# Performance work log

Measured on AMD Instinct MI355X. Metric: run time of the kernel, lower is better.

Reference implementation:

```python
import jax, jax.numpy as jnp
import numpy as np

T, B, L, CTX, H = 512, 512, 16, 64, 128
STATE_DIM, SHOT, PID, DATA = 32, 12, 35, 23


def setup_inputs() -> dict:
    key = jax.random.key(0)
    ks = jax.random.split(key, 64)
    k = iter(ks)
    def rn(shape, s=0.1):
        return (jax.random.normal(next(k), shape) * s).astype(jnp.float32)
    xs = jax.random.normal(next(k), (T, B, DATA), jnp.float32)
    xs = xs.at[:, :, 12].set(jax.random.randint(next(k), (T, B), 0, SHOT).astype(jnp.float32))
    xs = xs.at[:, :, 17].set(jax.random.randint(next(k), (T, B), 0, PID).astype(jnp.float32))
    xs = xs.at[:, :, 20].set(jax.random.randint(next(k), (T, B), 0, SHOT).astype(jnp.float32))
    return dict(
        total_xs=jnp.zeros((1,), jnp.float32),
        xs=xs,
        ts=jnp.linspace(0.0, 2.0, T).astype(jnp.float32),
        noise_std=jnp.asarray(0.1, jnp.float32),
        z0_noise=jax.random.normal(next(k), (B, L), jnp.float32),
        bm_noise=jax.random.normal(next(k), (T - 1, B, L), jnp.float32),
        shot_emb=rn((SHOT, 8)), player_emb=rn((PID, 8)),
        gru_wih=rn((3 * H, STATE_DIM)), gru_whh=rn((3 * H, H)),
        gru_bih=rn((3 * H,)), gru_bhh=rn((3 * H,)),
        enc_w=rn((CTX, H)), enc_b=rn((CTX,)),
        qz0_w=rn((2 * L, CTX)), qz0_b=rn((2 * L,)),
        f_w1=rn((H, L + CTX)), f_b1=rn((H,)), f_w2=rn((H, H)), f_b2=rn((H,)),
        f_w3=rn((L, H)), f_b3=rn((L,)),
        h_w1=rn((H, L)), h_b1=rn((H,)), h_w2=rn((H, H)), h_b2=rn((H,)),
        h_w3=rn((L, H)), h_b3=rn((L,)),
        g_w1=rn((L, H)), g_b1=rn((L, H)), g_w2=rn((L, H)), g_b2=rn((L,)),
        proj_w=rn((STATE_DIM, L)), proj_b=rn((STATE_DIM,)),
        pz0_mean=jnp.zeros((1, L), jnp.float32), pz0_logstd=jnp.zeros((1, L), jnp.float32),
        act_w=rn((128, L)), act_b=rn((128,)),
        act_land_w=rn((2, 128)), act_shot_w=rn((SHOT, 128)), act_move_w=rn((2, 128)),
    )


def _forward(xs, noise_std, shot_emb, player_emb, gru_wih, gru_whh, gru_bih, gru_bhh,
             enc_w, enc_b, qz0_w, qz0_b,
             f_w1, f_b1, f_w2, f_b2, f_w3, f_b3,
             h_w1, h_b1, h_w2, h_b2, h_w3, h_b3,
             g_w1, g_b1, g_w2, g_b2,
             proj_w, proj_b, pz0_mean, pz0_logstd,
             act_w, act_b, act_land_w, act_shot_w, act_move_w,
             ts, z0_noise, bm_noise):
    # --- SDE_embed_and_transform: replace shot/player id cols with embeddings ---
    state = xs[:, :, :18]
    shot_ids = state[:, :, 12].astype(jnp.int32)
    pid_ids = state[:, :, 17].astype(jnp.int32)
    state_t = jnp.concatenate([state[:, :, :12], shot_emb[shot_ids],
                               state[:, :, 13:17], player_emb[pid_ids]], axis=-1)  # (T,B,32)
    xs_t = jnp.concatenate([state_t, xs[:, :, 18:]], axis=-1)  # (T,B,37)
    # --- Encoder: GRU over time-reversed states, linear head, flip back ---
    def gru_step(h, xt):
        gi = xt @ gru_wih.T + gru_bih
        gh = h @ gru_whh.T + gru_bhh
        ir, iz, inn = jnp.split(gi, 3, axis=-1)
        hr, hz, hn = jnp.split(gh, 3, axis=-1)
        r = jax.nn.sigmoid(ir + hr)
        zg = jax.nn.sigmoid(iz + hz)
        n = jnp.tanh(inn + r * hn)
        hnew = (1.0 - zg) * n + zg * h
        return hnew, hnew
    h0 = jnp.zeros((xs.shape[1], gru_whh.shape[1]), xs.dtype)
    _, hs = jax.lax.scan(gru_step, h0, state_t[::-1])
    ctx = (hs @ enc_w.T + enc_b)[::-1]  # (T,B,CTX)
    # --- posterior z0 ---
    qm, qls = jnp.split(ctx[0] @ qz0_w.T + qz0_b, 2, axis=1)
    z0 = qm + jnp.exp(qls) * z0_noise
    # --- Euler-Maruyama with logqp; searchsorted(right) -> ctx[min(i+1,T-1)] = ctx[i+1] ---
    dts = ts[1:] - ts[:-1]  # (T-1,)
    dW = jnp.sqrt(dts)[:, None, None] * bm_noise
    ctx_steps = ctx[1:]
    def mlp3(x, w1, b1, w2, b2, w3, b3):
        h1 = jax.nn.softplus(x @ w1.T + b1)
        h2 = jax.nn.softplus(h1 @ w2.T + b2)
        return h2 @ w3.T + b3
    def g_diag(y):  # (B,L): per-latent-dim scalar nets, batched over L
        hg = jax.nn.softplus(y[:, :, None] * g_w1[None] + g_b1[None])  # (B,L,H)
        return jax.nn.sigmoid(jnp.einsum('blh,lh->bl', hg, g_w2) + g_b2)
    def sde_step(z, inp):
        c, dw, dt = inp
        f_val = mlp3(jnp.concatenate([z, c], axis=1), f_w1, f_b1, f_w2, f_b2, f_w3, f_b3)
        h_val = mlp3(z, h_w1, h_b1, h_w2, h_b2, h_w3, h_b3)
        g_val = g_diag(z)
        u = (f_val - h_val) / g_val
        logr = 0.5 * jnp.sum(u * u, axis=1) * dt
        z_new = z + f_val * dt + g_val * dw
        return z_new, (z_new, logr)
    _, (z_tail, log_ratio) = jax.lax.scan(sde_step, z0, (ctx_steps, dW, dts))
    zs = jnp.concatenate([z0[None], z_tail], axis=0)  # (T,B,L)
    _xs = zs @ proj_w.T + proj_b  # (T,B,32)
    # --- action model losses ---
    a = jax.nn.relu(zs @ act_w.T + act_b)
    land = (a @ act_land_w.T).reshape(-1, 2)
    shot_logits = (a @ act_shot_w.T).reshape(-1, act_shot_w.shape[0])
    move = (a @ act_move_w.T).reshape(-1, 2)
    true_actions = xs_t[:, :, -5:]
    true_land = true_actions[:, :, :2].reshape(-1, 2)
    true_move = true_actions[:, :, 3:].reshape(-1, 2)
    true_shot = true_actions[:, :, 2].astype(jnp.int32).reshape(-1)
    land_loss = jnp.mean((land - true_land) ** 2)
    move_loss = jnp.mean((move - true_move) ** 2)
    logp = jax.nn.log_softmax(shot_logits, axis=-1)
    picked = jnp.take_along_axis(logp, true_shot[:, None], axis=1)[:, 0]
    mask = (true_shot != 0).astype(logp.dtype)  # CrossEntropy ignore_index=0
    shot_loss = -jnp.sum(picked * mask) / jnp.maximum(jnp.sum(mask), 1.0)
    # --- reconstruction log-likelihood ---
    xs_state = xs_t[:, :, :STATE_DIM]
    LOG2PI = 1.8378770664093453
    log_pxs = jnp.mean(jnp.sum(
        -0.5 * ((xs_state - _xs) / noise_std) ** 2 - jnp.log(noise_std) - 0.5 * LOG2PI,
        axis=(0, 2)))
    # --- KL(q(z0) || p(z0)) ---
    var_q = jnp.exp(2.0 * qls)
    var_p = jnp.exp(2.0 * pz0_logstd)
    kl = pz0_logstd - qls + (var_q + (qm - pz0_mean) ** 2) / (2.0 * var_p) - 0.5
    logqp0 = jnp.mean(jnp.sum(kl, axis=1))
    logqp_path = jnp.mean(jnp.sum(log_ratio, axis=0))
    return log_pxs, logqp0 + logqp_path + land_loss + shot_loss + move_loss


def reference(total_xs, xs, ts, noise_std, z0_noise, bm_noise, shot_emb, player_emb,
              gru_wih, gru_whh, gru_bih, gru_bhh, enc_w, enc_b, qz0_w, qz0_b,
              f_w1, f_b1, f_w2, f_b2, f_w3, f_b3, h_w1, h_b1, h_w2, h_b2, h_w3, h_b3,
              g_w1, g_b1, g_w2, g_b2, proj_w, proj_b, pz0_mean, pz0_logstd,
              act_w, act_b, act_land_w, act_shot_w, act_move_w):
    return _forward(xs, noise_std, shot_emb, player_emb, gru_wih, gru_whh, gru_bih, gru_bhh,
                    enc_w, enc_b, qz0_w, qz0_b,
                    f_w1, f_b1, f_w2, f_b2, f_w3, f_b3,
                    h_w1, h_b1, h_w2, h_b2, h_w3, h_b3,
                    g_w1, g_b1, g_w2, g_b2,
                    proj_w, proj_b, pz0_mean, pz0_logstd,
                    act_w, act_b, act_land_w, act_shot_w, act_move_w,
                    ts, z0_noise, bm_noise)
```

## Files before the change

kernel.cpp:

```cpp
#include <hip/hip_runtime.h>
#include <cstdint>

typedef _Float16 f16;
typedef _Float16 f16x2 __attribute__((ext_vector_type(2)));

#define T_STEPS 512
#define B_SZ 512
#define LOG2PI 1.8378770664093453f

__device__ __forceinline__ uint32_t packh2(float a, float b) {
  f16x2 v; v[0] = (f16)a; v[1] = (f16)b;
  return __builtin_bit_cast(uint32_t, v);
}

__device__ __forceinline__ float fdot2(uint32_t a, uint32_t b, float c) {
#if defined(__AMDGCN__) && __has_builtin(__builtin_amdgcn_fdot2)
  return __builtin_amdgcn_fdot2(__builtin_bit_cast(f16x2, a),
                                __builtin_bit_cast(f16x2, b), c, false);
#else
  f16x2 x = __builtin_bit_cast(f16x2, a), y = __builtin_bit_cast(f16x2, b);
  return c + (float)x[0] * (float)y[0] + (float)x[1] * (float)y[1];
#endif
}

#define DOT4(acc, w0, w1, w2, w3, v)                                     \
  do {                                                                   \
    acc = fdot2((w0), (v).x, acc); acc = fdot2((w1), (v).y, acc);        \
    acc = fdot2((w2), (v).z, acc); acc = fdot2((w3), (v).w, acc);        \
  } while (0)

__device__ __forceinline__ float sigmoidf_(float x) {
  return 1.0f / (1.0f + __expf(-x));
}
__device__ __forceinline__ float tanhf_(float x) {
  float ax = fabsf(x);
  float t = __expf(-2.0f * ax);
  float r = (1.0f - t) / (1.0f + t);
  return copysignf(r, x);
}
__device__ __forceinline__ float softplusf_(float x) {
  return fmaxf(x, 0.0f) + __logf(1.0f + __expf(-fabsf(x)));
}

__global__ __launch_bounds__(256) void k_embed(
    const float* __restrict__ xs, const float* __restrict__ shot_emb,
    const float* __restrict__ player_emb, f16* __restrict__ state_t,
    float* __restrict__ accums) {
  if (blockIdx.x == 0 && threadIdx.x < 16) accums[threadIdx.x] = 0.0f;
  size_t idx = (size_t)blockIdx.x * 256 + threadIdx.x;
  const float* xp = xs + idx * 23;
  f16* op = state_t + idx * 32;
  int sid = (int)xp[12];
  int pid = (int)xp[17];
#pragma unroll
  for (int i = 0; i < 12; ++i) op[i] = (f16)xp[i];
  const float* se = shot_emb + sid * 8;
#pragma unroll
  for (int i = 0; i < 8; ++i) op[12 + i] = (f16)se[i];
#pragma unroll
  for (int i = 0; i < 4; ++i) op[20 + i] = (f16)xp[13 + i];
  const float* pe = player_emb + pid * 8;
#pragma unroll
  for (int i = 0; i < 8; ++i) op[24 + i] = (f16)pe[i];
}

__global__ __launch_bounds__(512) void k_gru(
    const f16* __restrict__ state_t, const float* __restrict__ wih,
    const float* __restrict__ whh, const float* __restrict__ bih,
    const float* __restrict__ bhh, const float* __restrict__ enc_w,
    const float* __restrict__ enc_b, const float* __restrict__ qz0_w,
    const float* __restrict__ qz0_b, const float* __restrict__ z0_noise,
    const float* __restrict__ pz0_mean, const float* __restrict__ pz0_logstd,
    f16* __restrict__ ctx, float* __restrict__ z0_out,
    float* __restrict__ accums) {
  __shared__ uint32_t s_x[2][16];
  __shared__ uint32_t s_h[2][64];
  __shared__ float s_gates[2 * 128 * 4];
  __shared__ float s_encp[2 * 64 * 2];
  __shared__ float s_ctx0[2][64];
  __shared__ float s_q[2][32];

  const int tid = threadIdx.x;
  const int bbase = blockIdx.x * 2;
  const uint32_t* stu = (const uint32_t*)state_t;

  uint32_t wA[64];
  uint32_t wB[16];
  float bias0 = 0.f, bias1 = 0.f, encbr = 0.f;

  if (tid < 256) {
    int g = tid >> 7, du = tid & 127;
    const float* whr = whh + (size_t)(g * 128 + du) * 128;
#pragma unroll
    for (int i = 0; i < 64; ++i) wA[i] = packh2(whr[2 * i], whr[2 * i + 1]);
    const float* wxr = wih + (size_t)(g * 128 + du) * 32;
#pragma unroll
    for (int i = 0; i < 16; ++i) wB[i] = packh2(wxr[2 * i], wxr[2 * i + 1]);
    bias0 = bih[g * 128 + du] + bhh[g * 128 + du];
  } else if (tid < 384) {
    int du = tid - 256;
    const float* whr = whh + (size_t)(256 + du) * 128;
#pragma unroll
    for (int i = 0; i < 64; ++i) wA[i] = packh2(whr[2 * i], whr[2 * i + 1]);
    const float* wxr = wih + (size_t)(256 + du) * 32;
#pragma unroll
    for (int i = 0; i < 16; ++i) wB[i] = packh2(wxr[2 * i], wxr[2 * i + 1]);
    bias0 = bih[256 + du];
    bias1 = bhh[256 + du];
  } else {
    int e = tid - 384, c = e & 63, ks = e >> 6;
    const float* wer = enc_w + (size_t)c * 128 + ks * 64;
#pragma unroll
    for (int i = 0; i < 32; ++i) wA[i] = packh2(wer[2 * i], wer[2 * i + 1]);
    encbr = enc_b[c];
  }

  if (tid < 128) s_h[tid >> 6][tid & 63] = 0u;
  if (tid < 32) {
    int b = tid >> 4, i = tid & 15;
    s_x[b][i] = stu[((size_t)(T_STEPS - 1) * B_SZ + bbase + b) * 16 + i];
  }
  float h_old = 0.0f;
  __syncthreads();

  for (int t = T_STEPS - 1; t >= 0; --t) {
    uint4 xpref = make_uint4(0, 0, 0, 0);
    if (tid < 256) {
      int g = tid >> 7, du = tid & 127;
#pragma unroll
      for (int b = 0; b < 2; ++b) {
        float a = bias0;
        const uint4* xq = (const uint4*)&s_x[b][0];
#pragma unroll
        for (int j = 0; j < 4; ++j) {
          uint4 v = xq[j];
          DOT4(a, wB[4 * j], wB[4 * j + 1], wB[4 * j + 2], wB[4 * j + 3], v);
        }
        const uint4* hq = (const uint4*)&s_h[b][0];
#pragma unroll
        for (int j = 0; j < 16; ++j) {
          uint4 v = hq[j];
          DOT4(a, wA[4 * j], wA[4 * j + 1], wA[4 * j + 2], wA[4 * j + 3], v);
        }
        s_gates[(b * 128 + du) * 4 + g] = a;
      }
    } else if (tid < 384) {
      int du = tid - 256;
#pragma unroll
      for (int b = 0; b < 2; ++b) {
        float aI = bias0, aH = bias1;
        const uint4* xq = (const uint4*)&s_x[b][0];
#pragma unroll
        for (int j = 0; j < 4; ++j) {
          uint4 v = xq[j];
          DOT4(aI, wB[4 * j], wB[4 * j + 1], wB[4 * j + 2], wB[4 * j + 3], v);
        }
        const uint4* hq = (const uint4*)&s_h[b][0];
#pragma unroll
        for (int j = 0; j < 16; ++j) {
          uint4 v = hq[j];
          DOT4(aH, wA[4 * j], wA[4 * j + 1], wA[4 * j + 2], wA[4 * j + 3], v);
        }
        s_gates[(b * 128 + du) * 4 + 2] = aI;
        s_gates[(b * 128 + du) * 4 + 3] = aH;
      }
    } else {
      int e = tid - 384, ks = e >> 6, cc = e & 63;
      (void)cc;
      if (t < T_STEPS - 1) {
#pragma unroll
        for (int b = 0; b < 2; ++b) {
          float a = 0.f;
          const uint4* hq = (const uint4*)&s_h[b][ks * 32];
#pragma unroll
          for (int j = 0; j < 8; ++j) {
            uint4 v = hq[j];
            DOT4(a, wA[4 * j], wA[4 * j + 1], wA[4 * j + 2], wA[4 * j + 3], v);
          }
          s_encp[(b * 64 + cc) * 2 + ks] = a;
        }
      }
      if (e < 8 && t > 0) {
        int b = e & 1, q = e >> 1;
        xpref = *(const uint4*)(stu +
                                ((size_t)(t - 1) * B_SZ + bbase + b) * 16 + q * 4);
      }
    }
    __syncthreads();
    if (tid < 256) {
      int b = tid >> 7, du = tid & 127;
      const float4 gt = *(const float4*)&s_gates[(b * 128 + du) * 4];
      float r = sigmoidf_(gt.x), zg = sigmoidf_(gt.y);
      float n = tanhf_(gt.z + r * gt.w);
      float hnew = (1.0f - zg) * n + zg * h_old;
      h_old = hnew;
      ((f16*)&s_h[b][0])[du] = (f16)hnew;
    } else if (tid >= 384) {
      int e = tid - 384, cc = e & 63, b = e >> 6;
      if (t < T_STEPS - 1) {
        float2 p = *(const float2*)&s_encp[(b * 64 + cc) * 2];
        ctx[((size_t)(t + 1) * B_SZ + bbase + b) * 64 + cc] =
            (f16)(p.x + p.y + encbr);
      }
      if (e < 8 && t > 0) {
        int b2 = e & 1, q = e >> 1;
        *(uint4*)&s_x[b2][q * 4] = xpref;
      }
    }
    __syncthreads();
  }

  if (tid >= 384) {
    int e = tid - 384, ks = e >> 6, cc = e & 63;
#pragma unroll
    for (int b = 0; b < 2; ++b) {
      float a = 0.f;
      const uint4* hq = (const uint4*)&s_h[b][ks * 32];
#pragma unroll
      for (int j = 0; j < 8; ++j) {
        uint4 v = hq[j];
        DOT4(a, wA[4 * j], wA[4 * j + 1], wA[4 * j + 2], wA[4 * j + 3], v);
      }
      s_encp[(b * 64 + cc) * 2 + ks] = a;
    }
  }
  __syncthreads();
  if (tid >= 384) {
    int e = tid - 384, cc = e & 63, b = e >> 6;
    float2 p = *(const float2*)&s_encp[(b * 64 + cc) * 2];
    float val = p.x + p.y + encbr;
    ctx[((size_t)bbase + b) * 64 + cc] = (f16)val;
    s_ctx0[b][cc] = val;
  }
  __syncthreads();
  if (tid < 64) {
    int b = tid >> 5, o = tid & 31;
    float acc = qz0_b[o];
#pragma unroll 8
    for (int k = 0; k < 64; ++k) acc += qz0_w[o * 64 + k] * s_ctx0[b][k];
    s_q[b][o] = acc;
  }
  __syncthreads();
  if (tid < 32) {
    int b = tid >> 4, l = tid & 15;
    int bg = bbase + b;
    float qm = s_q[b][l], qls = s_q[b][16 + l];
    float z0v = qm + __expf(qls) * z0_noise[bg * 16 + l];
    z0_out[bg * 16 + l] = z0v;
    float pm = pz0_mean[l], pls = pz0_logstd[l];
    float var_q = __expf(2.0f * qls);
    float var_p = __expf(2.0f * pls);
    float dm = qm - pm;
    float kl = pls - qls + (var_q + dm * dm) / (2.0f * var_p) - 0.5f;
    atomicAdd(&accums[5], kl);
  }
}

__global__ __launch_bounds__(512) void k_sde(
    const f16* __restrict__ ctx, const float* __restrict__ z0_in,
    const float* __restrict__ ts, const float* __restrict__ bm_noise,
    const float* __restrict__ fw1, const float* __restrict__ fb1,
    const float* __restrict__ fw2, const float* __restrict__ fb2,
    const float* __restrict__ fw3, const float* __restrict__ fb3,
    const float* __restrict__ hw1, const float* __restrict__ hb1,
    const float* __restrict__ hw2, const float* __restrict__ hb2,
    const float* __restrict__ hw3, const float* __restrict__ hb3,
    const float* __restrict__ gw1, const float* __restrict__ gb1,
    const float* __restrict__ gw2, const float* __restrict__ gb2,
    f16* __restrict__ zs, float* __restrict__ accums) {
  __shared__ uint32_t s_x2[2][40];
  __shared__ float s_zf[2][16];
  __shared__ uint32_t s_h1[2][2][64];
  __shared__ uint32_t s_h2[2][2][64];
  __shared__ float s_gp[256];
  __shared__ float s_dts[512];

  const int tid = threadIdx.x;
  const int bbase = blockIdx.x * 2;

  uint32_t uw[48];
  uint32_t wP2[32];
  uint32_t wP3[32];
  float bias1r = 0.f, bias2r = 0.f, gb2r = 0.f, fb3r = 0.f, hb3r = 0.f;

  if (tid < 256) {
    int l = tid & 15, k8 = (tid >> 4) & 7;
#pragma unroll
    for (int i = 0; i < 16; ++i) {
      int h = k8 * 16 + i;
      uw[i] = __builtin_bit_cast(uint32_t, gw1[l * 128 + h]);
      uw[16 + i] = __builtin_bit_cast(uint32_t, gb1[l * 128 + h]);
      uw[32 + i] = __builtin_bit_cast(uint32_t, gw2[l * 128 + h]);
    }
  } else if (tid < 384) {
    int u = tid - 256;
    const float* w = fw1 + (size_t)u * 80;
#pragma unroll
    for (int i = 0; i < 40; ++i) uw[i] = packh2(w[2 * i], w[2 * i + 1]);
    bias1r = fb1[u];
  } else {
    int u = tid - 384;
    const float* w = hw1 + (size_t)u * 16;
#pragma unroll
    for (int i = 0; i < 8; ++i) uw[i] = packh2(w[2 * i], w[2 * i + 1]);
    bias1r = hb1[u];
  }
  {
    int u = (tid >> 1) & 127, ks = tid & 1, mlp = tid >> 8;
    const float* w = (mlp ? hw2 : fw2) + (size_t)u * 128 + ks * 64;
#pragma unroll
    for (int i = 0; i < 32; ++i) wP2[i] = packh2(w[2 * i], w[2 * i + 1]);
    bias2r = (mlp ? hb2 : fb2)[u];
  }
  if (tid < 128) {
    int l = (tid >> 2) & 15, mlp = (tid >> 1) & 1, kh = tid & 1;
    const float* w = (mlp ? hw3 : fw3) + (size_t)l * 128 + kh * 64;
#pragma unroll
    for (int i = 0; i < 32; ++i) wP3[i] = packh2(w[2 * i], w[2 * i + 1]);
    if ((tid & 3) == 0) {
      gb2r = gb2[l];
      fb3r = fb3[l];
      hb3r = hb3[l];
    }
  }

  if (tid < 511) s_dts[tid] = ts[tid + 1] - ts[tid];
  float bmc = 0.f;
  float path_acc = 0.0f;
  uint4 cpref = make_uint4(0, 0, 0, 0);
  if (tid < 128 && (tid & 3) == 0) {
    int b = tid >> 6, l = (tid >> 2) & 15, bg = bbase + b;
    float z = z0_in[bg * 16 + l];
    s_zf[b][l] = z;
    ((f16*)&s_x2[b][0])[l] = (f16)z;
    zs[(size_t)bg * 16 + l] = (f16)z;
    bmc = bm_noise[((size_t)0 * B_SZ + bg) * 16 + l];
  }
  if (tid >= 128 && tid < 144) {
    int i = tid - 128, b = i & 1, q = i >> 1;
    const uint32_t* cu = (const uint32_t*)ctx;
    uint4 v = *(const uint4*)(cu + ((size_t)1 * B_SZ + bbase + b) * 32 + q * 4);
    *(uint4*)&s_x2[b][8 + q * 4] = v;
  }
  __syncthreads();

  for (int t = 0; t < T_STEPS - 1; ++t) {
    float bmn = 0.f;
    if (tid < 128 && (tid & 3) == 0 && t < T_STEPS - 2) {
      int b = tid >> 6, l = (tid >> 2) & 15;
      bmn = bm_noise[((size_t)(t + 1) * B_SZ + bbase + b) * 16 + l];
    }
    if (tid >= 128 && tid < 144 && t <= T_STEPS - 3) {
      int i = tid - 128, b = i & 1, q = i >> 1;
      const uint32_t* cu = (const uint32_t*)ctx;
      cpref = *(const uint4*)(cu +
                              ((size_t)(t + 2) * B_SZ + bbase + b) * 32 + q * 4);
    }
    if (tid < 256) {
      int b = tid >> 7, l = tid & 15, k8 = (tid >> 4) & 7;
      float y = s_zf[b][l];
      float acc = 0.f;
#pragma unroll
      for (int i = 0; i < 16; ++i) {
        float pre = fmaf(y, __builtin_bit_cast(float, uw[i]),
                         __builtin_bit_cast(float, uw[16 + i]));
        acc = fmaf(softplusf_(pre), __builtin_bit_cast(float, uw[32 + i]), acc);
      }
      s_gp[(b * 16 + l) * 8 + k8] = acc;
    } else if (tid < 384) {
      int u = tid - 256;
#pragma unroll
      for (int b = 0; b < 2; ++b) {
        float a0 = bias1r, a1 = 0.f;
        const uint4* xq = (const uint4*)&s_x2[b][0];
#pragma unroll
        for (int j = 0; j < 10; j += 2) {
          uint4 v0 = xq[j], v1 = xq[j + 1];
          DOT4(a0, uw[4 * j], uw[4 * j + 1], uw[4 * j + 2], uw[4 * j + 3], v0);
          DOT4(a1, uw[4 * j + 4], uw[4 * j + 5], uw[4 * j + 6], uw[4 * j + 7], v1);
        }
        ((f16*)&s_h1[0][b][0])[u] = (f16)softplusf_(a0 + a1);
      }
    } else {
      int u = tid - 384;
#pragma unroll
      for (int b = 0; b < 2; ++b) {
        float a = bias1r;
        const uint4* xq = (const uint4*)&s_x2[b][0];
#pragma unroll
        for (int j = 0; j < 2; ++j) {
          uint4 v = xq[j];
          DOT4(a, uw[4 * j], uw[4 * j + 1], uw[4 * j + 2], uw[4 * j + 3], v);
        }
        ((f16*)&s_h1[1][b][0])[u] = (f16)softplusf_(a);
      }
    }
    __syncthreads();
    {
      int u = (tid >> 1) & 127, ks = tid & 1, mlp = tid >> 8;
      float p0a = 0.f, p0b = 0.f, p1a = 0.f, p1b = 0.f;
      const uint4* h0q = (const uint4*)&s_h1[mlp][0][ks * 32];
      const uint4* h1q = (const uint4*)&s_h1[mlp][1][ks * 32];
#pragma unroll
      for (int j = 0; j < 8; j += 2) {
        uint4 v0 = h0q[j], v1 = h0q[j + 1];
        DOT4(p0a, wP2[4 * j], wP2[4 * j + 1], wP2[4 * j + 2], wP2[4 * j + 3], v0);
        DOT4(p0b, wP2[4 * j + 4], wP2[4 * j + 5], wP2[4 * j + 6], wP2[4 * j + 7], v1);
        uint4 w0 = h1q[j], w1 = h1q[j + 1];
        DOT4(p1a, wP2[4 * j], wP2[4 * j + 1], wP2[4 * j + 2], wP2[4 * j + 3], w0);
        DOT4(p1b, wP2[4 * j + 4], wP2[4 * j + 5], wP2[4 * j + 6], wP2[4 * j + 7], w1);
      }
      float p0 = p0a + p0b, p1 = p1a + p1b;
      p0 += __shfl_xor(p0, 1);
      p1 += __shfl_xor(p1, 1);
      float sel = ks ? p1 : p0;
      ((f16*)&s_h2[mlp][ks][0])[u] = (f16)softplusf_(sel + bias2r);
    }
    __syncthreads();
    if (tid < 128) {
      int b = tid >> 6, l = (tid >> 2) & 15, mlp = (tid >> 1) & 1, kh = tid & 1;
      const uint4* hq = (const uint4*)&s_h2[mlp][b][kh * 32];
      float a0 = 0.f, a1 = 0.f;
#pragma unroll
      for (int j = 0; j < 8; j += 2) {
        uint4 v0 = hq[j], v1 = hq[j + 1];
        DOT4(a0, wP3[4 * j], wP3[4 * j + 1], wP3[4 * j + 2], wP3[4 * j + 3], v0);
        DOT4(a1, wP3[4 * j + 4], wP3[4 * j + 5], wP3[4 * j + 6], wP3[4 * j + 7], v1);
      }
      float a = a0 + a1;
      float full = a + __shfl_xor(a, 1);
      float other = __shfl_xor(full, 2);
      if ((tid & 3) == 0) {
        float fv = full + fb3r;
        float hv = other + hb3r;
        const float4* gp = (const float4*)&s_gp[(b * 16 + l) * 8];
        float4 g0 = gp[0], g1 = gp[1];
        float gv = sigmoidf_(g0.x + g0.y + g0.z + g0.w +
                             g1.x + g1.y + g1.z + g1.w + gb2r);
        float dt = s_dts[t];
        float u_ = (fv - hv) / gv;
        float lsum = u_ * u_;
        lsum += __shfl_xor(lsum, 4);
        lsum += __shfl_xor(lsum, 8);
        lsum += __shfl_xor(lsum, 16);
        lsum += __shfl_xor(lsum, 32);
        if (l == 0) path_acc += 0.5f * lsum * dt;
        float dw = sqrtf(dt) * bmc;
        float zn = s_zf[b][l] + fv * dt + gv * dw;
        s_zf[b][l] = zn;
        ((f16*)&s_x2[b][0])[l] = (f16)zn;
        zs[((size_t)(t + 1) * B_SZ + bbase + b) * 16 + l] = (f16)zn;
        bmc = bmn;
      }
    } else if (tid >= 128 && tid < 144 && t <= T_STEPS - 3) {
      int i = tid - 128, b = i & 1, q = i >> 1;
      *(uint4*)&s_x2[b][8 + q * 4] = cpref;
    }
    __syncthreads();
  }
  if (tid == 0 || tid == 64) atomicAdd(&accums[6], path_acc);
}

__global__ __launch_bounds__(256) void k_dec(
    const f16* __restrict__ zs, const f16* __restrict__ state_t,
    const float* __restrict__ xs, const float* __restrict__ proj_w,
    const float* __restrict__ proj_b, const float* __restrict__ act_w,
    const float* __restrict__ act_b, const float* __restrict__ land_w,
    const float* __restrict__ shot_w, const float* __restrict__ move_w,
    float* __restrict__ accums) {
  __shared__ uint32_t s_proj[8 * 32];
  __shared__ uint32_t s_act[8 * 128];
  __shared__ uint32_t s_head[128 * 8];
  __shared__ float s_pb[32], s_ab[128];
  __shared__ float s_red[4 * 5];

  const int tid = threadIdx.x;
  for (int id = tid; id < 8 * 32; id += 256) {
    int kp = id & 7, n = id >> 3;
    s_proj[kp * 32 + n] = packh2(proj_w[n * 16 + 2 * kp], proj_w[n * 16 + 2 * kp + 1]);
  }
  for (int id = tid; id < 8 * 128; id += 256) {
    int kp = id & 7, n = id >> 3;
    s_act[kp * 128 + n] = packh2(act_w[n * 16 + 2 * kp], act_w[n * 16 + 2 * kp + 1]);
  }
  for (int id = tid; id < 128 * 8; id += 256) {
    int j = id >> 3, p = id & 7;
    int h0 = 2 * p, h1 = 2 * p + 1;
    float w0 = (h0 < 2) ? land_w[h0 * 128 + j]
                        : (h0 < 14 ? shot_w[(h0 - 2) * 128 + j]
                                   : move_w[(h0 - 14) * 128 + j]);
    float w1 = (h1 < 2) ? land_w[h1 * 128 + j]
                        : (h1 < 14 ? shot_w[(h1 - 2) * 128 + j]
                                   : move_w[(h1 - 14) * 128 + j]);
    s_head[j * 8 + p] = packh2(w0, w1);
  }
  if (tid < 32) s_pb[tid] = proj_b[tid];
  if (tid < 128) s_ab[tid] = act_b[tid];
  __syncthreads();

  size_t idx = (size_t)blockIdx.x * 256 + tid;
  uint32_t z2[8];
  const uint32_t* zp = (const uint32_t*)(zs + idx * 16);
#pragma unroll
  for (int i = 0; i < 8; ++i) z2[i] = zp[i];
  uint32_t stv[16];
  const uint32_t* stp = (const uint32_t*)(state_t + idx * 32);
#pragma unroll
  for (int i = 0; i < 16; ++i) stv[i] = stp[i];

  float sqsum = 0.0f;
#pragma unroll 4
  for (int i = 0; i < 32; ++i) {
    float acc = s_pb[i];
#pragma unroll
    for (int kp = 0; kp < 8; ++kp) acc = fdot2(s_proj[kp * 32 + i], z2[kp], acc);
    f16x2 sv = __builtin_bit_cast(f16x2, stv[i >> 1]);
    float d = (float)sv[i & 1] - acc;
    sqsum += d * d;
  }

  float hd[16];
#pragma unroll
  for (int i = 0; i < 16; ++i) hd[i] = 0.0f;
#pragma unroll 2
  for (int j = 0; j < 128; ++j) {
    float a = s_ab[j];
#pragma unroll
    for (int kp = 0; kp < 8; ++kp) a = fdot2(s_act[kp * 128 + j], z2[kp], a);
    a = fmaxf(a, 0.0f);
#pragma unroll
    for (int p = 0; p < 8; ++p) {
      f16x2 w = __builtin_bit_cast(f16x2, s_head[j * 8 + p]);
      hd[2 * p] += (float)w[0] * a;
      hd[2 * p + 1] += (float)w[1] * a;
    }
  }
  const float* xp = xs + idx * 23;
  float dl0 = hd[0] - xp[18], dl1 = hd[1] - xp[19];
  float land = dl0 * dl0 + dl1 * dl1;
  float dm0 = hd[14] - xp[21], dm1 = hd[15] - xp[22];
  float move = dm0 * dm0 + dm1 * dm1;
  int sid = (int)xp[20];
  float m = hd[2];
#pragma unroll
  for (int s = 1; s < 12; ++s) m = fmaxf(m, hd[2 + s]);
  float sume = 0.0f;
#pragma unroll
  for (int s = 0; s < 12; ++s) sume += __expf(hd[2 + s] - m);
  float lse = m + __logf(sume);
  float pl = 0.0f;
#pragma unroll
  for (int s = 0; s < 12; ++s)
    if (s == sid) pl = hd[2 + s];
  float picked = 0.0f, cnt = 0.0f;
  if (sid != 0) {
    picked = pl - lse;
    cnt = 1.0f;
  }
  float vals[5] = {sqsum, land, move, picked, cnt};
#pragma unroll
  for (int v = 0; v < 5; ++v) {
    float x = vals[v];
    for (int off = 1; off < 64; off <<= 1) x += __shfl_xor(x, off);
    vals[v] = x;
  }
  int lane = tid & 63, wv = tid >> 6;
  if (lane == 0) {
#pragma unroll
    for (int v = 0; v < 5; ++v) s_red[wv * 5 + v] = vals[v];
  }
  __syncthreads();
  if (tid == 0) {
#pragma unroll
    for (int v = 0; v < 5; ++v) {
      float s = s_red[v] + s_red[5 + v] + s_red[10 + v] + s_red[15 + v];
      atomicAdd(&accums[v], s);
    }
  }
}

__global__ void k_fin(const float* __restrict__ accums,
                      const float* __restrict__ noise_std,
                      float* __restrict__ out) {
  if (threadIdx.x == 0 && blockIdx.x == 0) {
    float sd = noise_std[0];
    float log_pxs = -0.5f * accums[0] / (sd * sd * (float)B_SZ) -
                    (float)T_STEPS * 32.0f * (logf(sd) + 0.5f * LOG2PI);
    float land = accums[1] / (float)(T_STEPS * B_SZ * 2);
    float move = accums[2] / (float)(T_STEPS * B_SZ * 2);
    float shot = -accums[3] / fmaxf(accums[4], 1.0f);
    float out1 = accums[5] / (float)B_SZ + accums[6] / (float)B_SZ + land + shot + move;
    out[0] = log_pxs;
    out[1] = out1;
  }
}

extern "C" void kernel_launch(void* const* d_in, const int* in_sizes, int n_in,
                              void* d_out, int out_size, void* d_ws,
                              size_t ws_size, hipStream_t stream) {
  const float* xs = (const float*)d_in[1];
  const float* ts = (const float*)d_in[2];
  const float* noise_std = (const float*)d_in[3];
  const float* z0_noise = (const float*)d_in[4];
  const float* bm_noise = (const float*)d_in[5];
  const float* shot_emb = (const float*)d_in[6];
  const float* player_emb = (const float*)d_in[7];
  const float* gru_wih = (const float*)d_in[8];
  const float* gru_whh = (const float*)d_in[9];
  const float* gru_bih = (const float*)d_in[10];
  const float* gru_bhh = (const float*)d_in[11];
  const float* enc_w = (const float*)d_in[12];
  const float* enc_b = (const float*)d_in[13];
  const float* qz0_w = (const float*)d_in[14];
  const float* qz0_b = (const float*)d_in[15];
  const float* f_w1 = (const float*)d_in[16];
  const float* f_b1 = (const float*)d_in[17];
  const float* f_w2 = (const float*)d_in[18];
  const float* f_b2 = (const float*)d_in[19];
  const float* f_w3 = (const float*)d_in[20];
  const float* f_b3 = (const float*)d_in[21];
  const float* h_w1 = (const float*)d_in[22];
  const float* h_b1 = (const float*)d_in[23];
  const float* h_w2 = (const float*)d_in[24];
  const float* h_b2 = (const float*)d_in[25];
  const float* h_w3 = (const float*)d_in[26];
  const float* h_b3 = (const float*)d_in[27];
  const float* g_w1 = (const float*)d_in[28];
  const float* g_b1 = (const float*)d_in[29];
  const float* g_w2 = (const float*)d_in[30];
  const float* g_b2 = (const float*)d_in[31];
  const float* proj_w = (const float*)d_in[32];
  const float* proj_b = (const float*)d_in[33];
  const float* pz0_mean = (const float*)d_in[34];
  const float* pz0_logstd = (const float*)d_in[35];
  const float* act_w = (const float*)d_in[36];
  const float* act_b = (const float*)d_in[37];
  const float* act_land_w = (const float*)d_in[38];
  const float* act_shot_w = (const float*)d_in[39];
  const float* act_move_w = (const float*)d_in[40];

  char* ws = (char*)d_ws;
  float* accums = (float*)ws;
  f16* state_t = (f16*)(ws + 256);
  f16* ctx = (f16*)(ws + 256 + 16777216);
  float* z0b = (float*)(ws + 256 + 16777216 + 33554432);
  f16* zs = (f16*)(ws + 256 + 16777216 + 33554432 + 32768);

  k_embed<<<1024, 256, 0, stream>>>(xs, shot_emb, player_emb, state_t, accums);
  k_gru<<<256, 512, 0, stream>>>(state_t, gru_wih, gru_whh, gru_bih, gru_bhh,
                                 enc_w, enc_b, qz0_w, qz0_b, z0_noise, pz0_mean,
                                 pz0_logstd, ctx, z0b, accums);
  k_sde<<<256, 512, 0, stream>>>(ctx, z0b, ts, bm_noise, f_w1, f_b1, f_w2, f_b2,
                                 f_w3, f_b3, h_w1, h_b1, h_w2, h_b2, h_w3, h_b3,
                                 g_w1, g_b1, g_w2, g_b2, zs, accums);
  k_dec<<<1024, 256, 0, stream>>>(zs, state_t, xs, proj_w, proj_b, act_w, act_b,
                                  act_land_w, act_shot_w, act_move_w, accums);
  k_fin<<<1, 64, 0, stream>>>(accums, noise_std, (float*)d_out);
}
```

Before: 1.986 ms.

## Restructure SDE kernel to one batch element per 256-thread block

The SDE integration kernel now runs one batch element per block with 256 threads and 512 blocks, instead of two elements per 512-thread block across 256 blocks. Each thread holds a full row of the second MLP layer in registers, so the split-K shuffle reduction goes away, and the g-network work is split into 16 chunks per latent dim. This puts more independent blocks across the CUs on the latency-bound sequential time loop. In exchange it uses more registers per thread and no longer shares weight loads across two batch elements.

```diff
diff --git a/kernel.cpp b/kernel.cpp
--- a/kernel.cpp
+++ b/kernel.cpp
@@ -256,7 +256,7 @@
   }
 }
 
-__global__ __launch_bounds__(512) void k_sde(
+__global__ __launch_bounds__(256, 2) void k_sde(
     const f16* __restrict__ ctx, const float* __restrict__ z0_in,
     const float* __restrict__ ts, const float* __restrict__ bm_noise,
     const float* __restrict__ fw1, const float* __restrict__ fb1,
@@ -268,52 +268,54 @@
     const float* __restrict__ gw1, const float* __restrict__ gb1,
     const float* __restrict__ gw2, const float* __restrict__ gb2,
     f16* __restrict__ zs, float* __restrict__ accums) {
-  __shared__ uint32_t s_x2[2][40];
-  __shared__ float s_zf[2][16];
-  __shared__ uint32_t s_h1[2][2][64];
-  __shared__ uint32_t s_h2[2][2][64];
+  __shared__ uint32_t s_x2[40];
+  __shared__ float s_zf[16];
+  __shared__ uint32_t s_h1[2][64];
+  __shared__ uint32_t s_h2[2][64];
   __shared__ float s_gp[256];
-  __shared__ float s_dts[512];
+  __shared__ float s_dts[T_STEPS];
 
   const int tid = threadIdx.x;
-  const int bbase = blockIdx.x * 2;
-
-  uint32_t uw[48];
-  uint32_t wP2[32];
+  const int bg = blockIdx.x;
+  const uint32_t* cu = (const uint32_t*)ctx;
+
+  uint32_t gw1r[8], gb1r[8], gw2r[8];
+  uint32_t uw1[40];
+  uint32_t wP2[64];
   uint32_t wP3[32];
   float bias1r = 0.f, bias2r = 0.f, gb2r = 0.f, fb3r = 0.f, hb3r = 0.f;
 
-  if (tid < 256) {
-    int l = tid & 15, k8 = (tid >> 4) & 7;
-#pragma unroll
-    for (int i = 0; i < 16; ++i) {
-      int h = k8 * 16 + i;
-      uw[i] = __builtin_bit_cast(uint32_t, gw1[l * 128 + h]);
-      uw[16 + i] = __builtin_bit_cast(uint32_t, gb1[l * 128 + h]);
-      uw[32 + i] = __builtin_bit_cast(uint32_t, gw2[l * 128 + h]);
-    }
-  } else if (tid < 384) {
-    int u = tid - 256;
-    const float* w = fw1 + (size_t)u * 80;
-#pragma unroll
-    for (int i = 0; i < 40; ++i) uw[i] = packh2(w[2 * i], w[2 * i + 1]);
-    bias1r = fb1[u];
+  {
+    int l = tid & 15, kc = tid >> 4;
+#pragma unroll
+    for (int i = 0; i < 8; ++i) {
+      int h = kc * 8 + i;
+      gw1r[i] = __builtin_bit_cast(uint32_t, gw1[l * 128 + h]);
+      gb1r[i] = __builtin_bit_cast(uint32_t, gb1[l * 128 + h]);
+      gw2r[i] = __builtin_bit_cast(uint32_t, gw2[l * 128 + h]);
+    }
+  }
+  if (tid < 128) {
+    const float* w = fw1 + (size_t)tid * 80;
+#pragma unroll
+    for (int i = 0; i < 40; ++i) uw1[i] = packh2(w[2 * i], w[2 * i + 1]);
+    bias1r = fb1[tid];
   } else {
-    int u = tid - 384;
+    int u = tid - 128;
     const float* w = hw1 + (size_t)u * 16;
 #pragma unroll
-    for (int i = 0; i < 8; ++i) uw[i] = packh2(w[2 * i], w[2 * i + 1]);
+    for (int i = 0; i < 8; ++i) uw1[i] = packh2(w[2 * i], w[2 * i + 1]);
     bias1r = hb1[u];
   }
   {
-    int u = (tid >> 1) & 127, ks = tid & 1, mlp = tid >> 8;
-    const float* w = (mlp ? hw2 : fw2) + (size_t)u * 128 + ks * 64;
-#pragma unroll
-    for (int i = 0; i < 32; ++i) wP2[i] = packh2(w[2 * i], w[2 * i + 1]);
+    int mlp = tid >> 7, u = tid & 127;
+    const float* w = (mlp ? hw2 : fw2) + (size_t)u * 128;
+#pragma unroll
+    for (int i = 0; i < 64; ++i) wP2[i] = packh2(w[2 * i], w[2 * i + 1]);
     bias2r = (mlp ? hb2 : fb2)[u];
   }
-  if (tid < 128) {
-    int l = (tid >> 2) & 15, mlp = (tid >> 1) & 1, kh = tid & 1;
+  if (tid < 64) {
+    int l = tid >> 2, mlp = (tid >> 1) & 1, kh = tid & 1;
     const float* w = (mlp ? hw3 : fw3) + (size_t)l * 128 + kh * 64;
 #pragma unroll
     for (int i = 0; i < 32; ++i) wP3[i] = packh2(w[2 * i], w[2 * i + 1]);
@@ -324,102 +326,83 @@
     }
   }
 
-  if (tid < 511) s_dts[tid] = ts[tid + 1] - ts[tid];
+  for (int i = tid; i < T_STEPS - 1; i += 256) s_dts[i] = ts[i + 1] - ts[i];
   float bmc = 0.f;
   float path_acc = 0.0f;
   uint4 cpref = make_uint4(0, 0, 0, 0);
-  if (tid < 128 && (tid & 3) == 0) {
-    int b = tid >> 6, l = (tid >> 2) & 15, bg = bbase + b;
+  if (tid < 64 && (tid & 3) == 0) {
+    int l = tid >> 2;
     float z = z0_in[bg * 16 + l];
-    s_zf[b][l] = z;
-    ((f16*)&s_x2[b][0])[l] = (f16)z;
+    s_zf[l] = z;
+    ((f16*)&s_x2[0])[l] = (f16)z;
     zs[(size_t)bg * 16 + l] = (f16)z;
-    bmc = bm_noise[((size_t)0 * B_SZ + bg) * 16 + l];
-  }
-  if (tid >= 128 && tid < 144) {
-    int i = tid - 128, b = i & 1, q = i >> 1;
-    const uint32_t* cu = (const uint32_t*)ctx;
-    uint4 v = *(const uint4*)(cu + ((size_t)1 * B_SZ + bbase + b) * 32 + q * 4);
-    *(uint4*)&s_x2[b][8 + q * 4] = v;
+    bmc = bm_noise[(size_t)bg * 16 + l];
+  }
+  if (tid >= 128 && tid < 136) {
+    int q = tid - 128;
+    uint4 v = *(const uint4*)(cu + ((size_t)1 * B_SZ + bg) * 32 + q * 4);
+    *(uint4*)&s_x2[8 + q * 4] = v;
   }
   __syncthreads();
 
   for (int t = 0; t < T_STEPS - 1; ++t) {
     float bmn = 0.f;
-    if (tid < 128 && (tid & 3) == 0 && t < T_STEPS - 2) {
-      int b = tid >> 6, l = (tid >> 2) & 15;
-      bmn = bm_noise[((size_t)(t + 1) * B_SZ + bbase + b) * 16 + l];
-    }
-    if (tid >= 128 && tid < 144 && t <= T_STEPS - 3) {
-      int i = tid - 128, b = i & 1, q = i >> 1;
-      const uint32_t* cu = (const uint32_t*)ctx;
-      cpref = *(const uint4*)(cu +
-                              ((size_t)(t + 2) * B_SZ + bbase + b) * 32 + q * 4);
-    }
-    if (tid < 256) {
-      int b = tid >> 7, l = tid & 15, k8 = (tid >> 4) & 7;
-      float y = s_zf[b][l];
+    if (tid < 64 && (tid & 3) == 0 && t < T_STEPS - 2)
+      bmn = bm_noise[((size_t)(t + 1) * B_SZ + bg) * 16 + (tid >> 2)];
+    if (tid >= 128 && tid < 136 && t <= T_STEPS - 3) {
+      int q = tid - 128;
+      cpref = *(const uint4*)(cu + ((size_t)(t + 2) * B_SZ + bg) * 32 + q * 4);
+    }
+    {
+      int l = tid & 15;
+      float y = s_zf[l];
       float acc = 0.f;
 #pragma unroll
-      for (int i = 0; i < 16; ++i) {
-        float pre = fmaf(y, __builtin_bit_cast(float, uw[i]),
-                         __builtin_bit_cast(float, uw[16 + i]));
-        acc = fmaf(softplusf_(pre), __builtin_bit_cast(float, uw[32 + i]), acc);
-      }
-      s_gp[(b * 16 + l) * 8 + k8] = acc;
-    } else if (tid < 384) {
-      int u = tid - 256;
-#pragma unroll
-      for (int b = 0; b < 2; ++b) {
-        float a0 = bias1r, a1 = 0.f;
-        const uint4* xq = (const uint4*)&s_x2[b][0];
-#pragma unroll
-        for (int j = 0; j < 10; j += 2) {
-          uint4 v0 = xq[j], v1 = xq[j + 1];
-          DOT4(a0, uw[4 * j], uw[4 * j + 1], uw[4 * j + 2], uw[4 * j + 3], v0);
-          DOT4(a1, uw[4 * j + 4], uw[4 * j + 5], uw[4 * j + 6], uw[4 * j + 7], v1);
-        }
-        ((f16*)&s_h1[0][b][0])[u] = (f16)softplusf_(a0 + a1);
-      }
+      for (int i = 0; i < 8; ++i) {
+        float pre = fmaf(y, __builtin_bit_cast(float, gw1r[i]),
+                         __builtin_bit_cast(float, gb1r[i]));
+        acc = fmaf(softplusf_(pre), __builtin_bit_cast(float, gw2r[i]), acc);
+      }
+      s_gp[l * 16 + (tid >> 4)] = acc;
+    }
+    if (tid < 128) {
+      float a0 = bias1r, a1 = 0.f;
+      const uint4* xq = (const uint4*)&s_x2[0];
+#pragma unroll
+      for (int j = 0; j < 10; j += 2) {
+        uint4 v0 = xq[j], v1 = xq[j + 1];
+        DOT4(a0, uw1[4 * j], uw1[4 * j + 1], uw1[4 * j + 2], uw1[4 * j + 3], v0);
+        DOT4(a1, uw1[4 * j + 4], uw1[4 * j + 5], uw1[4 * j + 6], uw1[4 * j + 7], v1);
+      }
+      ((f16*)&s_h1[0][0])[tid] = (f16)softplusf_(a0 + a1);
     } else {
-      int u = tid - 384;
-#pragma unroll
-      for (int b = 0; b < 2; ++b) {
-        float a = bias1r;
-        const uint4* xq = (const uint4*)&s_x2[b][0];
-#pragma unroll
-        for (int j = 0; j < 2; ++j) {
-          uint4 v = xq[j];
-          DOT4(a, uw[4 * j], uw[4 * j + 1], uw[4 * j + 2], uw[4 * j + 3], v);
-        }
-        ((f16*)&s_h1[1][b][0])[u] = (f16)softplusf_(a);
-      }
+      float a = bias1r;
+      const uint4* xq = (const uint4*)&s_x2[0];
+#pragma unroll
+      for (int j = 0; j < 2; ++j) {
+        uint4 v = xq[j];
+        DOT4(a, uw1[4 * j], uw1[4 * j + 1], uw1[4 * j + 2], uw1[4 * j + 3], v);
+      }
+      ((f16*)&s_h1[1][0])[tid - 128] = (f16)softplusf_(a);
     }
     __syncthreads();
     {
-      int u = (tid >> 1) & 127, ks = tid & 1, mlp = tid >> 8;
-      float p0a = 0.f, p0b = 0.f, p1a = 0.f, p1b = 0.f;
-      const uint4* h0q = (const uint4*)&s_h1[mlp][0][ks * 32];
-      const uint4* h1q = (const uint4*)&s_h1[mlp][1][ks * 32];
-#pragma unroll
-      for (int j = 0; j < 8; j += 2) {
-        uint4 v0 = h0q[j], v1 = h0q[j + 1];
-        DOT4(p0a, wP2[4 * j], wP2[4 * j + 1], wP2[4 * j + 2], wP2[4 * j + 3], v0);
-        DOT4(p0b, wP2[4 * j + 4], wP2[4 * j + 5], wP2[4 * j + 6], wP2[4 * j + 7], v1);
-        uint4 w0 = h1q[j], w1 = h1q[j + 1];
-        DOT4(p1a, wP2[4 * j], wP2[4 * j + 1], wP2[4 * j + 2], wP2[4 * j + 3], w0);
-        DOT4(p1b, wP2[4 * j + 4], wP2[4 * j + 5], wP2[4 * j + 6], wP2[4 * j + 7], w1);
-      }
-      float p0 = p0a + p0b, p1 = p1a + p1b;
-      p0 += __shfl_xor(p0, 1);
-      p1 += __shfl_xor(p1, 1);
-      float sel = ks ? p1 : p0;
-      ((f16*)&s_h2[mlp][ks][0])[u] = (f16)softplusf_(sel + bias2r);
+      int mlp = tid >> 7, u = tid & 127;
+      float a0 = 0.f, a1 = 0.f;
+      const uint4* hq = (const uint4*)&s_h1[mlp][0];
+#pragma unroll
+      for (int j = 0; j < 16; j += 2) {
+        uint4 v0 = hq[j], v1 = hq[j + 1];
+        DOT4(a0, wP2[4 * j], wP2[4 * j + 1], wP2[4 * j + 2], wP2[4 * j + 3], v0);
+        DOT4(a1, wP2[4 * j + 4], wP2[4 * j + 5], wP2[4 * j + 6], wP2[4 * j + 7], v1);
+      }
+      ((f16*)&s_h2[mlp][0])[u] = (f16)softplusf_(a0 + a1 + bias2r);
     }
     __syncthreads();
-    if (tid < 128) {
-      int b = tid >> 6, l = (tid >> 2) & 15, mlp = (tid >> 1) & 1, kh = tid & 1;
-      const uint4* hq = (const uint4*)&s_h2[mlp][b][kh * 32];
+    if (tid < 64) {
+      int l = tid >> 2, kh = tid & 1;
+      int mlp = (tid >> 1) & 1;
+      const uint4* hq = (const uint4*)&s_h2[mlp][kh * 32];
       float a0 = 0.f, a1 = 0.f;
 #pragma unroll
       for (int j = 0; j < 8; j += 2) {
@@ -433,10 +416,11 @@
       if ((tid & 3) == 0) {
         float fv = full + fb3r;
         float hv = other + hb3r;
-        const float4* gp = (const float4*)&s_gp[(b * 16 + l) * 8];
-        float4 g0 = gp[0], g1 = gp[1];
-        float gv = sigmoidf_(g0.x + g0.y + g0.z + g0.w +
-                             g1.x + g1.y + g1.z + g1.w + gb2r);
+        const float4* gp = (const float4*)&s_gp[l * 16];
+        float4 g0 = gp[0], g1 = gp[1], g2 = gp[2], g3 = gp[3];
+        float gs = g0.x + g0.y + g0.z + g0.w + g1.x + g1.y + g1.z + g1.w +
+                   g2.x + g2.y + g2.z + g2.w + g3.x + g3.y + g3.z + g3.w + gb2r;
+        float gv = sigmoidf_(gs);
         float dt = s_dts[t];
         float u_ = (fv - hv) / gv;
         float lsum = u_ * u_;
@@ -444,21 +428,21 @@
         lsum += __shfl_xor(lsum, 8);
         lsum += __shfl_xor(lsum, 16);
         lsum += __shfl_xor(lsum, 32);
-        if (l == 0) path_acc += 0.5f * lsum * dt;
+        if (tid == 0) path_acc += 0.5f * lsum * dt;
         float dw = sqrtf(dt) * bmc;
-        float zn = s_zf[b][l] + fv * dt + gv * dw;
-        s_zf[b][l] = zn;
-        ((f16*)&s_x2[b][0])[l] = (f16)zn;
-        zs[((size_t)(t + 1) * B_SZ + bbase + b) * 16 + l] = (f16)zn;
+        float zn = s_zf[l] + fv * dt + gv * dw;
+        s_zf[l] = zn;
+        ((f16*)&s_x2[0])[l] = (f16)zn;
+        zs[((size_t)(t + 1) * B_SZ + bg) * 16 + l] = (f16)zn;
         bmc = bmn;
       }
-    } else if (tid >= 128 && tid < 144 && t <= T_STEPS - 3) {
-      int i = tid - 128, b = i & 1, q = i >> 1;
-      *(uint4*)&s_x2[b][8 + q * 4] = cpref;
+    } else if (tid >= 128 && tid < 136 && t <= T_STEPS - 3) {
+      int q = tid - 128;
+      *(uint4*)&s_x2[8 + q * 4] = cpref;
     }
     __syncthreads();
   }
-  if (tid == 0 || tid == 64) atomicAdd(&accums[6], path_acc);
+  if (tid == 0) atomicAdd(&accums[6], path_acc);
 }
 
 __global__ __launch_bounds__(256) void k_dec(
@@ -650,7 +634,7 @@
   k_gru<<<256, 512, 0, stream>>>(state_t, gru_wih, gru_whh, gru_bih, gru_bhh,
                                  enc_w, enc_b, qz0_w, qz0_b, z0_noise, pz0_mean,
                                  pz0_logstd, ctx, z0b, accums);
-  k_sde<<<256, 512, 0, stream>>>(ctx, z0b, ts, bm_noise, f_w1, f_b1, f_w2, f_b2,
+  k_sde<<<512, 256, 0, stream>>>(ctx, z0b, ts, bm_noise, f_w1, f_b1, f_w2, f_b2,
                                  f_w3, f_b3, h_w1, h_b1, h_w2, h_b2, h_w3, h_b3,
                                  g_w1, g_b1, g_w2, g_b2, zs, accums);
   k_dec<<<1024, 256, 0, stream>>>(zs, state_t, xs, proj_w, proj_b, act_w, act_b,
```

Result: faster. 1.923 ms (-3.2%).
